# Optimization experiments

Measured on AMD Instinct MI355X. Metric: run time of the kernel, lower is better.

The kernel has to match this reference:

```python
import jax, jax.numpy as jnp
import numpy as np

N_NODES = 100000
N_EDGES = 3200000
IN_DIM = 256
HID_DIM = 64
OUT_DIM = 64


def setup_inputs() -> dict:
    key = jax.random.key(0)
    k1, k2, k3, k4, k5, k6 = jax.random.split(key, 6)
    x = jax.random.normal(k1, (N_NODES, IN_DIM), dtype=jnp.float32)
    edge_index = jax.random.randint(k2, (2, N_EDGES), 0, N_NODES, dtype=jnp.int32)
    # Glorot-style init for the two GCNConv layers (PyG default: glorot weight, zero bias)
    W1 = jax.random.normal(k3, (IN_DIM, HID_DIM), dtype=jnp.float32) * (1.0 / np.sqrt(IN_DIM))
    b1 = jnp.zeros((HID_DIM,), dtype=jnp.float32)
    W2 = jax.random.normal(k4, (HID_DIM, OUT_DIM), dtype=jnp.float32) * (1.0 / np.sqrt(HID_DIM))
    b2 = jnp.zeros((OUT_DIM,), dtype=jnp.float32)
    return {"x": x, "edge_index": edge_index, "W1": W1, "b1": b1, "W2": W2, "b2": b2}


def _gcn_conv(x, src, dst, deg_inv_sqrt, W, b, n):
    # PyG GCNConv: h = x W; out_i = sum_j norm_ij * h_j + b, with symmetric norm
    h = x @ W                                   # (n, d_out) small GEMM
    norm = deg_inv_sqrt[src] * deg_inv_sqrt[dst]  # (E+n,)
    msg = norm[:, None] * h[src]                # gather (E+n, d_out)
    agg = jax.ops.segment_sum(msg, dst, num_segments=n)  # scatter-add
    return agg + b


def reference(x, edge_index, W1, b1, W2, b2):
    n = x.shape[0]
    loops = jnp.arange(n, dtype=edge_index.dtype)
    src = jnp.concatenate([edge_index[0], loops])
    dst = jnp.concatenate([edge_index[1], loops])
    # degree on destination (col) with added self-loops, weight 1.0
    deg = jax.ops.segment_sum(jnp.ones_like(dst, dtype=x.dtype), dst, num_segments=n)
    deg_inv_sqrt = jnp.where(deg > 0, jax.lax.rsqrt(deg), 0.0)
    h = jax.nn.relu(_gcn_conv(x, src, dst, deg_inv_sqrt, W1, b1, n))
    return _gcn_conv(h, src, dst, deg_inv_sqrt, W2, b2, n)
```

## Files before the change

### kernel.cpp

```cpp
#include <hip/hip_runtime.h>
#include <cstdint>
#include <cstddef>


#define BIN_SHIFT 7
#define BIN_NODES 128
#define MAX_BINS 1024
#define SUP_SHIFT 11
#define FINE_PER_SUP 16
#define NSUP_MAX 64
#define SCAP 56
#define SRC_BITS 17
#define SRC_MASK ((1 << SRC_BITS) - 1)

typedef unsigned short ushort_t;

__device__ __forceinline__ float4 bfq2f4(uint2 p) {
  float4 r;
  r.x = __uint_as_float(p.x << 16);
  r.y = __uint_as_float(p.x & 0xFFFF0000u);
  r.z = __uint_as_float(p.y << 16);
  r.w = __uint_as_float(p.y & 0xFFFF0000u);
  return r;
}
__device__ __forceinline__ unsigned f2bf(float f) {
  unsigned u = __float_as_uint(f);
  return (u + 0x7FFFu + ((u >> 16) & 1u)) >> 16;
}
__device__ __forceinline__ uint2 f42bfq(float4 f) {
  uint2 r;
  r.x = f2bf(f.x) | (f2bf(f.y) << 16);
  r.y = f2bf(f.z) | (f2bf(f.w) << 16);
  return r;
}

__global__ void zero_int(int* __restrict__ p, int n) {
  int i = blockIdx.x * blockDim.x + threadIdx.x;
  if (i < n) p[i] = 0;
}

__global__ __launch_bounds__(256) void bin_count(const int* __restrict__ dst, int E, int nbins,
                                                 int* __restrict__ binCnt) {
  __shared__ int h[MAX_BINS];
  for (int i = threadIdx.x; i < nbins; i += 256) h[i] = 0;
  __syncthreads();
  int stride = gridDim.x * 256;
  for (int e = blockIdx.x * 256 + threadIdx.x; e < E; e += stride)
    atomicAdd(&h[dst[e] >> BIN_SHIFT], 1);
  __syncthreads();
  for (int i = threadIdx.x; i < nbins; i += 256)
    if (h[i]) atomicAdd(&binCnt[i], h[i]);
}

__global__ __launch_bounds__(256) void bin_scan(const int* __restrict__ binCnt, int nbins, int E,
                                                int* __restrict__ binStart,
                                                int* __restrict__ binCursor,
                                                int* __restrict__ supCursor) {
  __shared__ int s[256];
  int t = threadIdx.x;
  int c[4];
  int sum = 0;
#pragma unroll
  for (int i = 0; i < 4; i++) {
    int idx = t * 4 + i;
    c[i] = (idx < nbins) ? binCnt[idx] : 0;
    sum += c[i];
  }
  int v = sum;
  s[t] = v;
  __syncthreads();
  for (int d = 1; d < 256; d <<= 1) {
    int add = (t >= d) ? s[t - d] : 0;
    __syncthreads();
    s[t] += add;
    __syncthreads();
  }
  int run = s[t] - v;
#pragma unroll
  for (int i = 0; i < 4; i++) {
    int idx = t * 4 + i;
    if (idx < nbins) {
      binStart[idx] = run;
      binCursor[idx] = run;
      if ((idx & (FINE_PER_SUP - 1)) == 0) supCursor[idx >> 4] = run;
      run += c[i];
    }
  }
  if (t == 0) binStart[nbins] = E;
}

__global__ __launch_bounds__(256) void super_fill(const int* __restrict__ src,
                                                  const int* __restrict__ dst, int E, int nsup,
                                                  int* __restrict__ supCursor,
                                                  unsigned* __restrict__ supbuf) {
  __shared__ unsigned stage[NSUP_MAX * SCAP];
  __shared__ int lcnt[NSUP_MAX], lbase[NSUP_MAX], lscan[NSUP_MAX + 1];
  int chunk = (E + gridDim.x - 1) / gridDim.x;
  int c0 = blockIdx.x * chunk;
  int c1 = min(E, c0 + chunk);
  for (int t0 = c0; t0 < c1; t0 += 2048) {
    int t1 = min(c1, t0 + 2048);
    if (threadIdx.x < nsup) lcnt[threadIdx.x] = 0;
    __syncthreads();
    for (int e = t0 + threadIdx.x; e < t1; e += 256) {
      int d = dst[e];
      int sb = d >> SUP_SHIFT;
      unsigned v = ((unsigned)(d & ((1 << SUP_SHIFT) - 1)) << SRC_BITS) | (unsigned)src[e];
      int idx = atomicAdd(&lcnt[sb], 1);
      if (idx < SCAP)
        stage[sb * SCAP + idx] = v;
      else {
        int g = atomicAdd(&supCursor[sb], 1);
        supbuf[g] = v;
      }
    }
    __syncthreads();
    if (threadIdx.x < nsup) {
      int c = min(lcnt[threadIdx.x], SCAP);
      lcnt[threadIdx.x] = c;
      lbase[threadIdx.x] = c ? atomicAdd(&supCursor[threadIdx.x], c) : 0;
    }
    __syncthreads();
    if (threadIdx.x == 0) {
      int r = 0;
      for (int i = 0; i < nsup; i++) {
        lscan[i] = r;
        r += lcnt[i];
      }
      lscan[nsup] = r;
    }
    __syncthreads();
    int total = lscan[nsup];
    for (int j = threadIdx.x; j < total; j += 256) {
      int lo = 0, hi = nsup;
      while (hi - lo > 1) {
        int mid = (lo + hi) >> 1;
        if (lscan[mid] <= j)
          lo = mid;
        else
          hi = mid;
      }
      int off = j - lscan[lo];
      supbuf[lbase[lo] + off] = stage[lo * SCAP + off];
    }
    __syncthreads();
  }
}

__global__ __launch_bounds__(256) void fine_fill(const unsigned* __restrict__ supbuf,
                                                 const int* __restrict__ binStart, int nbins,
                                                 int* __restrict__ binCursor,
                                                 unsigned* __restrict__ binbuf) {
  __shared__ int lcnt[FINE_PER_SUP], lbase[FINE_PER_SUP];
  int sb = blockIdx.x >> 3, p = blockIdx.x & 7;
  int seg0 = binStart[sb << 4];
  int seg1 = binStart[min((sb + 1) << 4, nbins)];
  int part = (seg1 - seg0 + 7) >> 3;
  int c0 = seg0 + p * part;
  int c1 = min(seg1, c0 + part);
  if (threadIdx.x < FINE_PER_SUP) lcnt[threadIdx.x] = 0;
  __syncthreads();
  for (int i = c0 + threadIdx.x; i < c1; i += 256) atomicAdd(&lcnt[supbuf[i] >> 24], 1);
  __syncthreads();
  if (threadIdx.x < FINE_PER_SUP) {
    int c = lcnt[threadIdx.x];
    lbase[threadIdx.x] = c ? atomicAdd(&binCursor[(sb << 4) + threadIdx.x], c) : 0;
    lcnt[threadIdx.x] = 0;
  }
  __syncthreads();
  for (int i = c0 + threadIdx.x; i < c1; i += 256) {
    unsigned v = supbuf[i];
    unsigned dls = v >> SRC_BITS;
    int f = dls >> BIN_SHIFT;
    unsigned vf = ((dls & (BIN_NODES - 1)) << SRC_BITS) | (v & SRC_MASK);
    int idx = lbase[f] + atomicAdd(&lcnt[f], 1);
    binbuf[idx] = vf;
  }
}

__global__ __launch_bounds__(256) void node_count_dis(const unsigned* __restrict__ binbuf,
                                                      const int* __restrict__ binStart, int N,
                                                      int* __restrict__ count,
                                                      float* __restrict__ dis) {
  __shared__ int cnt[BIN_NODES];
  int b = blockIdx.x;
  int nodeBase = b << BIN_SHIFT;
  if (threadIdx.x < BIN_NODES) cnt[threadIdx.x] = 0;
  __syncthreads();
  int s0 = binStart[b], s1 = binStart[b + 1];
  for (int i = s0 + threadIdx.x; i < s1; i += 256) atomicAdd(&cnt[binbuf[i] >> SRC_BITS], 1);
  __syncthreads();
  if (threadIdx.x < BIN_NODES) {
    int node = nodeBase + threadIdx.x;
    if (node < N) {
      int c = cnt[threadIdx.x];
      count[node] = c;
      dis[node] = rsqrtf((float)(c + 1));
    }
  }
}

__global__ __launch_bounds__(256) void bin_csr(const unsigned* __restrict__ binbuf,
                                               const int* __restrict__ binStart,
                                               const int* __restrict__ count, int N, int E,
                                               int* __restrict__ rowptr, int* __restrict__ col) {
  __shared__ int cur[BIN_NODES];
  __shared__ int pref[BIN_NODES];
  int b = blockIdx.x, t = threadIdx.x;
  int nodeBase = b << BIN_SHIFT;
  int c = 0;
  if (t < BIN_NODES) {
    int node = nodeBase + t;
    c = (node < N) ? count[node] : 0;
    pref[t] = c;
  }
  __syncthreads();
  for (int d = 1; d < BIN_NODES; d <<= 1) {
    int add = (t < BIN_NODES && t >= d) ? pref[t - d] : 0;
    __syncthreads();
    if (t < BIN_NODES) pref[t] += add;
    __syncthreads();
  }
  int s0 = binStart[b];
  if (t < BIN_NODES) {
    int node = nodeBase + t;
    if (node < N) {
      int ex = s0 + pref[t] - c;
      rowptr[node] = ex;
      cur[t] = ex;
    }
  }
  if (b == 0 && t == 255) rowptr[N] = E;
  __syncthreads();
  int s1 = binStart[b + 1];
  for (int i = s0 + t; i < s1; i += 256) {
    unsigned v = binbuf[i];
    int slot = atomicAdd(&cur[v >> SRC_BITS], 1);
    col[slot] = v & SRC_MASK;
  }
}

template <int K, bool ABF16>
__global__ __launch_bounds__(256, 4) void gemm64(const void* __restrict__ Av,
                                                 const float* __restrict__ W,
                                                 uint2* __restrict__ Cb, int M) {
  constexpr int CHUNK = (K > 128) ? 128 : K;
  __shared__ float4 wlds[CHUNK * 16];

  const int c0 = threadIdx.x & 15;
  const int rq = threadIdx.x >> 4;
  const int r0 = blockIdx.x * 64 + rq * 4;

  float4 acc[4];
#pragma unroll
  for (int i = 0; i < 4; i++) acc[i] = make_float4(0.f, 0.f, 0.f, 0.f);
  size_t aoff[4];
  bool ok[4];
#pragma unroll
  for (int i = 0; i < 4; i++) {
    int r = r0 + i;
    ok[i] = (r < M);
    aoff[i] = (size_t)(ok[i] ? r : (M - 1)) * K;
  }

  for (int kc = 0; kc < K; kc += CHUNK) {
    {
      const float4* W4 = (const float4*)W + (size_t)kc * 16;
      for (int i = threadIdx.x; i < CHUNK * 16; i += 256) wlds[i] = W4[i];
    }
    __syncthreads();

#pragma unroll 2
    for (int k = 0; k < CHUNK; k += 4) {
      float4 xv[4];
#pragma unroll
      for (int i = 0; i < 4; i++) {
        size_t idx = aoff[i] + kc + k;
        if (ABF16)
          xv[i] = bfq2f4(*(const uint2*)((const ushort_t*)Av + idx));
        else
          xv[i] = *(const float4*)((const float*)Av + idx);
      }
      float4 w0 = wlds[(k + 0) * 16 + c0];
      float4 w1 = wlds[(k + 1) * 16 + c0];
      float4 w2 = wlds[(k + 2) * 16 + c0];
      float4 w3 = wlds[(k + 3) * 16 + c0];
#pragma unroll
      for (int i = 0; i < 4; i++) {
        acc[i].x += xv[i].x * w0.x + xv[i].y * w1.x + xv[i].z * w2.x + xv[i].w * w3.x;
        acc[i].y += xv[i].x * w0.y + xv[i].y * w1.y + xv[i].z * w2.y + xv[i].w * w3.y;
        acc[i].z += xv[i].x * w0.z + xv[i].y * w1.z + xv[i].z * w2.z + xv[i].w * w3.z;
        acc[i].w += xv[i].x * w0.w + xv[i].y * w1.w + xv[i].z * w2.w + xv[i].w * w3.w;
      }
    }
    __syncthreads();
  }
#pragma unroll
  for (int i = 0; i < 4; i++)
    if (ok[i]) Cb[(size_t)(r0 + i) * 16 + c0] = f42bfq(acc[i]);
}

template <bool OUTBF>
__global__ __launch_bounds__(256) void agg_kernel(
    const uint2* __restrict__ h, const int* __restrict__ rowptr, const int* __restrict__ col,
    const float* __restrict__ dis, const float* __restrict__ bias, void* __restrict__ outv,
    int N, int relu) {
  int wid = (blockIdx.x * blockDim.x + threadIdx.x) >> 6;
  if (wid >= N) return;
  int lane = threadIdx.x & 63;
  int sub = lane & 15;
  int quarter = lane >> 4;

  int start = rowptr[wid], end = rowptr[wid + 1];
  float di = dis[wid];

  float4 a0 = make_float4(0.f, 0.f, 0.f, 0.f), a1 = a0, a2 = a0, a3 = a0;
  {
    float4 self = bfq2f4(h[(size_t)wid * 16 + sub]);
    if (quarter == 0) {
      a0.x = di * self.x;
      a0.y = di * self.y;
      a0.z = di * self.z;
      a0.w = di * self.w;
    }
  }

  for (int base = start; base < end; base += 64) {
    int e = base + lane;
    int sj = 0;
    float wj = 0.f;
    if (e < end) {
      sj = col[e];
      wj = dis[sj];
    }
    int cnt = end - base;
    if (cnt > 64) cnt = 64;
    int rounds = (cnt + 3) >> 2;
    int t = 0;
    for (; t + 4 <= rounds; t += 4) {
      int i0 = 4 * t + quarter;
      int s0 = __shfl(sj, i0), s1 = __shfl(sj, i0 + 4), s2 = __shfl(sj, i0 + 8),
          s3 = __shfl(sj, i0 + 12);
      float w0 = __shfl(wj, i0), w1 = __shfl(wj, i0 + 4), w2 = __shfl(wj, i0 + 8),
            w3 = __shfl(wj, i0 + 12);
      float4 g0 = bfq2f4(h[(size_t)s0 * 16 + sub]);
      float4 g1 = bfq2f4(h[(size_t)s1 * 16 + sub]);
      float4 g2 = bfq2f4(h[(size_t)s2 * 16 + sub]);
      float4 g3 = bfq2f4(h[(size_t)s3 * 16 + sub]);
      a0.x += w0 * g0.x; a0.y += w0 * g0.y; a0.z += w0 * g0.z; a0.w += w0 * g0.w;
      a1.x += w1 * g1.x; a1.y += w1 * g1.y; a1.z += w1 * g1.z; a1.w += w1 * g1.w;
      a2.x += w2 * g2.x; a2.y += w2 * g2.y; a2.z += w2 * g2.z; a2.w += w2 * g2.w;
      a3.x += w3 * g3.x; a3.y += w3 * g3.y; a3.z += w3 * g3.z; a3.w += w3 * g3.w;
    }
    for (; t < rounds; t++) {
      int i0 = 4 * t + quarter;
      int s0 = __shfl(sj, i0);
      float w0 = __shfl(wj, i0);
      float4 g0 = bfq2f4(h[(size_t)s0 * 16 + sub]);
      a0.x += w0 * g0.x; a0.y += w0 * g0.y; a0.z += w0 * g0.z; a0.w += w0 * g0.w;
    }
  }

  float sx = (a0.x + a1.x) + (a2.x + a3.x);
  float sy = (a0.y + a1.y) + (a2.y + a3.y);
  float sz = (a0.z + a1.z) + (a2.z + a3.z);
  float sw = (a0.w + a1.w) + (a2.w + a3.w);
  sx += __shfl_down(sx, 32); sy += __shfl_down(sy, 32);
  sz += __shfl_down(sz, 32); sw += __shfl_down(sw, 32);
  sx += __shfl_down(sx, 16); sy += __shfl_down(sy, 16);
  sz += __shfl_down(sz, 16); sw += __shfl_down(sw, 16);
  if (quarter == 0) {
    float4 bv = ((const float4*)bias)[sub];
    float4 o = make_float4(di * sx + bv.x, di * sy + bv.y, di * sz + bv.z, di * sw + bv.w);
    if (relu) {
      o.x = fmaxf(o.x, 0.f);
      o.y = fmaxf(o.y, 0.f);
      o.z = fmaxf(o.z, 0.f);
      o.w = fmaxf(o.w, 0.f);
    }
    if (OUTBF)
      ((uint2*)outv)[(size_t)wid * 16 + sub] = f42bfq(o);
    else
      ((float4*)outv)[(size_t)wid * 16 + sub] = o;
  }
}

extern "C" void kernel_launch(void* const* d_in, const int* in_sizes, int n_in,
                              void* d_out, int out_size, void* d_ws, size_t ws_size,
                              hipStream_t stream) {
  const float* x = (const float*)d_in[0];
  const int* ei = (const int*)d_in[1];
  const float* W1 = (const float*)d_in[2];
  const float* b1 = (const float*)d_in[3];
  const float* W2 = (const float*)d_in[4];
  const float* b2 = (const float*)d_in[5];

  const int IN = 256;
  const int E = in_sizes[1] / 2;
  const int N = in_sizes[0] / IN;
  const int* src = ei;
  const int* dst = ei + E;
  const int nbins = (N + BIN_NODES - 1) >> BIN_SHIFT;
  const int nsup = (N + (1 << SUP_SHIFT) - 1) >> SUP_SHIFT;

  char* ws = (char*)d_ws;
  size_t off = 0;
  auto alloc = [&](size_t bytes) -> void* {
    void* p = ws + off;
    off += (bytes + 255) & ~(size_t)255;
    return p;
  };
  int* count = (int*)alloc((size_t)N * 4);
  int* rowptr = (int*)alloc((size_t)(N + 1) * 4);
  float* dis = (float*)alloc((size_t)N * 4);
  int* binCnt = (int*)alloc(MAX_BINS * 4);
  int* binStart = (int*)alloc((MAX_BINS + 1) * 4);
  int* binCursor = (int*)alloc(MAX_BINS * 4);
  int* supCursor = (int*)alloc(NSUP_MAX * 4);
  int* col = (int*)alloc((size_t)E * 4);
  unsigned* supbuf = (unsigned*)col;
  uint2* out1 = (uint2*)alloc((size_t)N * 64 * 2);
  size_t big = ((size_t)E * 4 > (size_t)N * 128) ? (size_t)E * 4 : (size_t)N * 128;
  unsigned* binbuf = (unsigned*)alloc(big);
  uint2* h = (uint2*)binbuf;
  float* outf = (float*)d_out;

  zero_int<<<(nbins + 255) / 256, 256, 0, stream>>>(binCnt, nbins);
  bin_count<<<1024, 256, 0, stream>>>(dst, E, nbins, binCnt);
  bin_scan<<<1, 256, 0, stream>>>(binCnt, nbins, E, binStart, binCursor, supCursor);
  super_fill<<<512, 256, 0, stream>>>(src, dst, E, nsup, supCursor, supbuf);
  fine_fill<<<nsup * 8, 256, 0, stream>>>(supbuf, binStart, nbins, binCursor, binbuf);
  node_count_dis<<<nbins, 256, 0, stream>>>(binbuf, binStart, N, count, dis);
  bin_csr<<<nbins, 256, 0, stream>>>(binbuf, binStart, count, N, E, rowptr, col);

  gemm64<256, false><<<(N + 63) / 64, 256, 0, stream>>>(x, W1, h, N);
  agg_kernel<true><<<(N + 3) / 4, 256, 0, stream>>>(h, rowptr, col, dis, b1, out1, N, 1);
  gemm64<64, true><<<(N + 63) / 64, 256, 0, stream>>>(out1, W2, h, N);
  agg_kernel<false><<<(N + 3) / 4, 256, 0, stream>>>(h, rowptr, col, dis, b2, outf, N, 0);
}
```

Measured before the change: 508.1 us.

## Merge fine binning, degree count and CSR fill into one per-bin kernel

```diff
diff --git a/kernel.cpp b/kernel.cpp
--- a/kernel.cpp
+++ b/kernel.cpp
@@ -7,9 +7,9 @@
 #define BIN_NODES 128
 #define MAX_BINS 1024
 #define SUP_SHIFT 11
-#define FINE_PER_SUP 16
 #define NSUP_MAX 64
-#define SCAP 56
+#define SCAP 120
+#define SF_TILE 3072
 #define SRC_BITS 17
 #define SRC_MASK ((1 << SRC_BITS) - 1)
 
@@ -39,8 +39,8 @@
   if (i < n) p[i] = 0;
 }
 
-__global__ __launch_bounds__(256) void bin_count(const int* __restrict__ dst, int E, int nbins,
-                                                 int* __restrict__ binCnt) {
+__global__ __launch_bounds__(256) void fine_count(const int* __restrict__ dst, int E, int nbins,
+                                                  int* __restrict__ binCnt) {
   __shared__ int h[MAX_BINS];
   for (int i = threadIdx.x; i < nbins; i += 256) h[i] = 0;
   __syncthreads();
@@ -54,7 +54,6 @@
 
 __global__ __launch_bounds__(256) void bin_scan(const int* __restrict__ binCnt, int nbins, int E,
                                                 int* __restrict__ binStart,
-                                                int* __restrict__ binCursor,
                                                 int* __restrict__ supCursor) {
   __shared__ int s[256];
   int t = threadIdx.x;
@@ -81,8 +80,7 @@
     int idx = t * 4 + i;
     if (idx < nbins) {
       binStart[idx] = run;
-      binCursor[idx] = run;
-      if ((idx & (FINE_PER_SUP - 1)) == 0) supCursor[idx >> 4] = run;
+      if ((idx & 15) == 0) supCursor[idx >> 4] = run;
       run += c[i];
     }
   }
@@ -95,123 +93,74 @@
                                                   unsigned* __restrict__ supbuf) {
   __shared__ unsigned stage[NSUP_MAX * SCAP];
   __shared__ int lcnt[NSUP_MAX], lbase[NSUP_MAX], lscan[NSUP_MAX + 1];
-  int chunk = (E + gridDim.x - 1) / gridDim.x;
-  int c0 = blockIdx.x * chunk;
-  int c1 = min(E, c0 + chunk);
-  for (int t0 = c0; t0 < c1; t0 += 2048) {
-    int t1 = min(c1, t0 + 2048);
-    if (threadIdx.x < nsup) lcnt[threadIdx.x] = 0;
-    __syncthreads();
-    for (int e = t0 + threadIdx.x; e < t1; e += 256) {
-      int d = dst[e];
-      int sb = d >> SUP_SHIFT;
-      unsigned v = ((unsigned)(d & ((1 << SUP_SHIFT) - 1)) << SRC_BITS) | (unsigned)src[e];
-      int idx = atomicAdd(&lcnt[sb], 1);
-      if (idx < SCAP)
-        stage[sb * SCAP + idx] = v;
-      else {
-        int g = atomicAdd(&supCursor[sb], 1);
-        supbuf[g] = v;
-      }
-    }
-    __syncthreads();
-    if (threadIdx.x < nsup) {
-      int c = min(lcnt[threadIdx.x], SCAP);
-      lcnt[threadIdx.x] = c;
-      lbase[threadIdx.x] = c ? atomicAdd(&supCursor[threadIdx.x], c) : 0;
-    }
-    __syncthreads();
-    if (threadIdx.x == 0) {
-      int r = 0;
-      for (int i = 0; i < nsup; i++) {
-        lscan[i] = r;
-        r += lcnt[i];
-      }
-      lscan[nsup] = r;
-    }
-    __syncthreads();
-    int total = lscan[nsup];
-    for (int j = threadIdx.x; j < total; j += 256) {
-      int lo = 0, hi = nsup;
-      while (hi - lo > 1) {
-        int mid = (lo + hi) >> 1;
-        if (lscan[mid] <= j)
-          lo = mid;
-        else
-          hi = mid;
-      }
-      int off = j - lscan[lo];
-      supbuf[lbase[lo] + off] = stage[lo * SCAP + off];
-    }
-    __syncthreads();
-  }
-}
-
-__global__ __launch_bounds__(256) void fine_fill(const unsigned* __restrict__ supbuf,
-                                                 const int* __restrict__ binStart, int nbins,
-                                                 int* __restrict__ binCursor,
-                                                 unsigned* __restrict__ binbuf) {
-  __shared__ int lcnt[FINE_PER_SUP], lbase[FINE_PER_SUP];
-  int sb = blockIdx.x >> 3, p = blockIdx.x & 7;
-  int seg0 = binStart[sb << 4];
-  int seg1 = binStart[min((sb + 1) << 4, nbins)];
-  int part = (seg1 - seg0 + 7) >> 3;
-  int c0 = seg0 + p * part;
-  int c1 = min(seg1, c0 + part);
-  if (threadIdx.x < FINE_PER_SUP) lcnt[threadIdx.x] = 0;
-  __syncthreads();
-  for (int i = c0 + threadIdx.x; i < c1; i += 256) atomicAdd(&lcnt[supbuf[i] >> 24], 1);
-  __syncthreads();
-  if (threadIdx.x < FINE_PER_SUP) {
-    int c = lcnt[threadIdx.x];
-    lbase[threadIdx.x] = c ? atomicAdd(&binCursor[(sb << 4) + threadIdx.x], c) : 0;
-    lcnt[threadIdx.x] = 0;
-  }
-  __syncthreads();
-  for (int i = c0 + threadIdx.x; i < c1; i += 256) {
-    unsigned v = supbuf[i];
-    unsigned dls = v >> SRC_BITS;
-    int f = dls >> BIN_SHIFT;
-    unsigned vf = ((dls & (BIN_NODES - 1)) << SRC_BITS) | (v & SRC_MASK);
-    int idx = lbase[f] + atomicAdd(&lcnt[f], 1);
-    binbuf[idx] = vf;
-  }
-}
-
-__global__ __launch_bounds__(256) void node_count_dis(const unsigned* __restrict__ binbuf,
-                                                      const int* __restrict__ binStart, int N,
-                                                      int* __restrict__ count,
-                                                      float* __restrict__ dis) {
-  __shared__ int cnt[BIN_NODES];
-  int b = blockIdx.x;
-  int nodeBase = b << BIN_SHIFT;
-  if (threadIdx.x < BIN_NODES) cnt[threadIdx.x] = 0;
-  __syncthreads();
-  int s0 = binStart[b], s1 = binStart[b + 1];
-  for (int i = s0 + threadIdx.x; i < s1; i += 256) atomicAdd(&cnt[binbuf[i] >> SRC_BITS], 1);
-  __syncthreads();
-  if (threadIdx.x < BIN_NODES) {
-    int node = nodeBase + threadIdx.x;
-    if (node < N) {
-      int c = cnt[threadIdx.x];
-      count[node] = c;
-      dis[node] = rsqrtf((float)(c + 1));
-    }
-  }
-}
-
-__global__ __launch_bounds__(256) void bin_csr(const unsigned* __restrict__ binbuf,
-                                               const int* __restrict__ binStart,
-                                               const int* __restrict__ count, int N, int E,
-                                               int* __restrict__ rowptr, int* __restrict__ col) {
+  int c0 = blockIdx.x * SF_TILE;
+  int c1 = min(E, c0 + SF_TILE);
+  if (threadIdx.x < nsup) lcnt[threadIdx.x] = 0;
+  __syncthreads();
+  for (int e = c0 + threadIdx.x; e < c1; e += 256) {
+    int d = dst[e];
+    int sb = d >> SUP_SHIFT;
+    unsigned v = ((unsigned)(d & ((1 << SUP_SHIFT) - 1)) << SRC_BITS) | (unsigned)src[e];
+    int idx = atomicAdd(&lcnt[sb], 1);
+    if (idx < SCAP)
+      stage[sb * SCAP + idx] = v;
+    else {
+      int g = atomicAdd(&supCursor[sb], 1);
+      supbuf[g] = v;
+    }
+  }
+  __syncthreads();
+  if (threadIdx.x < nsup) {
+    int c = min(lcnt[threadIdx.x], SCAP);
+    lcnt[threadIdx.x] = c;
+    lbase[threadIdx.x] = c ? atomicAdd(&supCursor[threadIdx.x], c) : 0;
+  }
+  __syncthreads();
+  if (threadIdx.x == 0) {
+    int r = 0;
+    for (int i = 0; i < nsup; i++) {
+      lscan[i] = r;
+      r += lcnt[i];
+    }
+    lscan[nsup] = r;
+  }
+  __syncthreads();
+  int total = lscan[nsup];
+  for (int j = threadIdx.x; j < total; j += 256) {
+    int lo = 0, hi = nsup;
+    while (hi - lo > 1) {
+      int mid = (lo + hi) >> 1;
+      if (lscan[mid] <= j)
+        lo = mid;
+      else
+        hi = mid;
+    }
+    int off = j - lscan[lo];
+    supbuf[lbase[lo] + off] = stage[lo * SCAP + off];
+  }
+}
+
+__global__ __launch_bounds__(256) void bin_csr2(const unsigned* __restrict__ supbuf,
+                                                const int* __restrict__ binStart, int nbins,
+                                                int N, int E, int* __restrict__ rowptr,
+                                                float* __restrict__ dis, int* __restrict__ col) {
   __shared__ int cur[BIN_NODES];
   __shared__ int pref[BIN_NODES];
   int b = blockIdx.x, t = threadIdx.x;
+  int sb = b >> 4, myf = b & 15;
   int nodeBase = b << BIN_SHIFT;
+  int seg0 = binStart[sb << 4];
+  int seg1 = binStart[min((sb + 1) << 4, nbins)];
+  if (t < BIN_NODES) cur[t] = 0;
+  __syncthreads();
+  for (int i = seg0 + t; i < seg1; i += 256) {
+    unsigned dls = supbuf[i] >> SRC_BITS;
+    if ((int)(dls >> BIN_SHIFT) == myf) atomicAdd(&cur[dls & (BIN_NODES - 1)], 1);
+  }
+  __syncthreads();
   int c = 0;
   if (t < BIN_NODES) {
-    int node = nodeBase + t;
-    c = (node < N) ? count[node] : 0;
+    c = cur[t];
     pref[t] = c;
   }
   __syncthreads();
@@ -221,22 +170,25 @@
     if (t < BIN_NODES) pref[t] += add;
     __syncthreads();
   }
-  int s0 = binStart[b];
+  int base = binStart[b];
   if (t < BIN_NODES) {
     int node = nodeBase + t;
     if (node < N) {
-      int ex = s0 + pref[t] - c;
+      int ex = base + pref[t] - c;
       rowptr[node] = ex;
       cur[t] = ex;
+      dis[node] = rsqrtf((float)(c + 1));
     }
   }
   if (b == 0 && t == 255) rowptr[N] = E;
   __syncthreads();
-  int s1 = binStart[b + 1];
-  for (int i = s0 + t; i < s1; i += 256) {
-    unsigned v = binbuf[i];
-    int slot = atomicAdd(&cur[v >> SRC_BITS], 1);
-    col[slot] = v & SRC_MASK;
+  for (int i = seg0 + t; i < seg1; i += 256) {
+    unsigned v = supbuf[i];
+    unsigned dls = v >> SRC_BITS;
+    if ((int)(dls >> BIN_SHIFT) == myf) {
+      int slot = atomicAdd(&cur[dls & (BIN_NODES - 1)], 1);
+      col[slot] = v & SRC_MASK;
+    }
   }
 }
 
@@ -244,7 +196,7 @@
 __global__ __launch_bounds__(256, 4) void gemm64(const void* __restrict__ Av,
                                                  const float* __restrict__ W,
                                                  uint2* __restrict__ Cb, int M) {
-  constexpr int CHUNK = (K > 128) ? 128 : K;
+  constexpr int CHUNK = (K > 64) ? 64 : K;
   __shared__ float4 wlds[CHUNK * 16];
 
   const int c0 = threadIdx.x & 15;
@@ -410,28 +362,25 @@
     off += (bytes + 255) & ~(size_t)255;
     return p;
   };
-  int* count = (int*)alloc((size_t)N * 4);
   int* rowptr = (int*)alloc((size_t)(N + 1) * 4);
   float* dis = (float*)alloc((size_t)N * 4);
   int* binCnt = (int*)alloc(MAX_BINS * 4);
   int* binStart = (int*)alloc((MAX_BINS + 1) * 4);
-  int* binCursor = (int*)alloc(MAX_BINS * 4);
   int* supCursor = (int*)alloc(NSUP_MAX * 4);
   int* col = (int*)alloc((size_t)E * 4);
-  unsigned* supbuf = (unsigned*)col;
   uint2* out1 = (uint2*)alloc((size_t)N * 64 * 2);
   size_t big = ((size_t)E * 4 > (size_t)N * 128) ? (size_t)E * 4 : (size_t)N * 128;
-  unsigned* binbuf = (unsigned*)alloc(big);
-  uint2* h = (uint2*)binbuf;
+  unsigned* supbuf = (unsigned*)alloc(big);
+  uint2* h = (uint2*)supbuf;
   float* outf = (float*)d_out;
 
+  const int nblkSF = (E + SF_TILE - 1) / SF_TILE;
+
   zero_int<<<(nbins + 255) / 256, 256, 0, stream>>>(binCnt, nbins);
-  bin_count<<<1024, 256, 0, stream>>>(dst, E, nbins, binCnt);
-  bin_scan<<<1, 256, 0, stream>>>(binCnt, nbins, E, binStart, binCursor, supCursor);
-  super_fill<<<512, 256, 0, stream>>>(src, dst, E, nsup, supCursor, supbuf);
-  fine_fill<<<nsup * 8, 256, 0, stream>>>(supbuf, binStart, nbins, binCursor, binbuf);
-  node_count_dis<<<nbins, 256, 0, stream>>>(binbuf, binStart, N, count, dis);
-  bin_csr<<<nbins, 256, 0, stream>>>(binbuf, binStart, count, N, E, rowptr, col);
+  fine_count<<<512, 256, 0, stream>>>(dst, E, nbins, binCnt);
+  bin_scan<<<1, 256, 0, stream>>>(binCnt, nbins, E, binStart, supCursor);
+  super_fill<<<nblkSF, 256, 0, stream>>>(src, dst, E, nsup, supCursor, supbuf);
+  bin_csr2<<<nbins, 256, 0, stream>>>(supbuf, binStart, nbins, N, E, rowptr, dis, col);
 
   gemm64<256, false><<<(N + 63) / 64, 256, 0, stream>>>(x, W1, h, N);
   agg_kernel<true><<<(N + 3) / 4, 256, 0, stream>>>(h, rowptr, col, dis, b1, out1, N, 1);
```

New measurement: 604.2 us. +18.9%, slower.
